# Performance work log

Hardware: AMD Instinct MI355X
Metric: run time of the kernel (lower is better)

The kernel has to match this reference:

```python
import jax, jax.numpy as jnp
import numpy as np


def _orthogonalize(Wfree):
    # Wfree: (S, C, C) free parameters -> batched QR with sign correction
    Q, R = jnp.linalg.qr(Wfree)
    s = jnp.sign(jnp.diagonal(R, axis1=-2, axis2=-1))  # (S, C)
    s = jnp.where(s == 0, jnp.ones_like(s), s)
    return Q * s[:, None, :]  # column-wise sign fix


def _channel_mix(x, Wfree):
    # x: (B, C, H, W); Wfree: (H*W, C, C)
    B, C, H, Wd = x.shape
    S = H * Wd
    Q = _orthogonalize(Wfree)                      # (S, C, C)
    xr = x.reshape(B, C, S).transpose(0, 2, 1)     # (B, S, C)
    # y[b,s,:] = x[b,s,:] @ Q[s].T  (matches torch matmul(x, Q.T))
    y = jnp.einsum('bsk,sck->bsc', xr, Q)
    return y.transpose(0, 2, 1).reshape(B, C, H, Wd)


def setup_inputs() -> dict:
    key = jax.random.key(0)
    k0, k1, k2, k3 = jax.random.split(key, 4)
    init_scale = 0.001
    x0 = jax.random.normal(k0, (32, 64, 28, 28), dtype=jnp.float32)
    x1 = jax.random.normal(k1, (32, 256, 14, 14), dtype=jnp.float32)
    W0 = jax.random.normal(k2, (28 * 28, 64, 64), dtype=jnp.float32) * init_scale
    W1 = jax.random.normal(k3, (14 * 14, 256, 256), dtype=jnp.float32) * init_scale
    return {"x0": x0, "x1": x1, "W0": W0, "W1": W1}


def reference(x0, x1, W0, W1):
    # C=64 and C=256 are perfect squares, so channel padding is a no-op.
    y0 = _channel_mix(x0, W0)
    y1 = _channel_mix(x1, W1)
    return (y0, y1)
```

## Files before the change

### kernel.cpp

```cpp
#include <hip/hip_runtime.h>


static constexpr int BB = 32;

#define SCHED_FENCE() __builtin_amdgcn_sched_barrier(0)

template<int CTRL>
__device__ __forceinline__ float dpp_add(float x) {
    int y = __builtin_amdgcn_update_dpp(0, __float_as_int(x), CTRL, 0xF, 0xF, false);
    return x + __int_as_float(y);
}
__device__ __forceinline__ float rowred16(float p) {
    p = dpp_add<0x128>(p);
    p = dpp_add<0x124>(p);
    p = dpp_add<0x122>(p);
    p = dpp_add<0x121>(p);
    return p;
}

__device__ __forceinline__ int qoff(int j, int g, int r16) {
    return j * 256 + g * 64 + ((r16 ^ (2 * g)) << 2);
}

__global__ __launch_bounds__(256) void tkern(const float* __restrict__ in,
                                             float* __restrict__ out,
                                             int R, int S) {
    __shared__ float tile[32][33];
    const int tx = threadIdx.x, ty = threadIdx.y;
    const int s0 = blockIdx.x * 32, r0 = blockIdx.y * 32;
    #pragma unroll
    for (int i = ty; i < 32; i += 8) {
        int r = r0 + i, s = s0 + tx;
        tile[i][tx] = (r < R && s < S) ? in[(size_t)r * S + s] : 0.f;
    }
    __syncthreads();
    #pragma unroll
    for (int i = ty; i < 32; i += 8) {
        int s = s0 + i, r = r0 + tx;
        if (s < S && r < R) out[(size_t)s * R + r] = tile[tx][i];
    }
}

template<int C, int CT, int KC>
__device__ __forceinline__ void qr_body(const float* __restrict__ W,
                                        float* __restrict__ XY,
                                        float* __restrict__ sm, int t) {
    constexpr int RT = 16;
    constexpr int TR = C / RT;
    constexpr int THREADS = RT * CT;
    constexpr int QSTR = TR + 4;
    constexpr int XSTR = C + 4;

    float* qs = sm;
    float* xs = sm + 2 * RT * QSTR;
    float* qc = xs + BB * XSTR;

    const int rb = t & 15;
    const int cb = t >> 4;

    float a[TR][4];
    {
        const float* Wp = W + (size_t)(rb * TR) * C + cb * 4;
        #pragma unroll
        for (int i = 0; i < TR; ++i) {
            float4 v = *reinterpret_cast<const float4*>(Wp + (size_t)i * C);
            a[i][0] = v.x; a[i][1] = v.y; a[i][2] = v.z; a[i][3] = v.w;
        }
    }
    {
        #pragma unroll
        for (int v = 0; v < (BB * C) / (4 * THREADS); ++v) {
            int idx = 4 * (t + v * THREADS);
            int b = idx / C, k = idx % C;
            float4 x4 = *reinterpret_cast<const float4*>(XY + idx);
            *reinterpret_cast<float4*>(&xs[b * XSTR + k]) = x4;
        }
    }

    int buf = 0;
    #pragma unroll 1
    for (int j = 0; j < C; ++j) {
        const int cbj = j >> 2, jj = j & 3;
        if (cb == cbj) {
            #pragma unroll
            for (int q = 0; q < 4; ++q) {
                if (q == jj) {
                    float p = 0.f;
                    #pragma unroll
                    for (int i = 0; i < TR; ++i) p += a[i][q] * a[i][q];
                    p = rowred16(p);
                    const float rn = 1.0f / sqrtf(p);
                    #pragma unroll
                    for (int i = 0; i < TR; ++i) a[i][q] *= rn;
                    #pragma unroll
                    for (int i = 0; i < TR; i += 4) {
                        *reinterpret_cast<float4*>(&qs[buf * RT * QSTR + rb * QSTR + i]) =
                            make_float4(a[i][q], a[i+1][q], a[i+2][q], a[i+3][q]);
                    }
                }
            }
        }
        __syncthreads();
        if (cb * 4 + 3 > j) {
            float qv[TR];
            #pragma unroll
            for (int i = 0; i < TR; i += 4) {
                float4 v = *reinterpret_cast<const float4*>(&qs[buf * RT * QSTR + rb * QSTR + i]);
                qv[i] = v.x; qv[i+1] = v.y; qv[i+2] = v.z; qv[i+3] = v.w;
            }
            #pragma unroll
            for (int q = 0; q < 4; ++q) {
                if (cb * 4 + q > j) {
                    float p = 0.f;
                    #pragma unroll
                    for (int i = 0; i < TR; ++i) p += a[i][q] * qv[i];
                    p = rowred16(p);
                    #pragma unroll
                    for (int i = 0; i < TR; ++i) a[i][q] -= p * qv[i];
                }
            }
        }
        buf ^= 1;
    }

    const int u  = t % (C / 4);
    const int bp = t / (C / 4);
    float acc[2][4] = {{0,0,0,0},{0,0,0,0}};

    #pragma unroll 1
    for (int ch = 0; ch < C / KC; ++ch) {
        __syncthreads();
        if (cb >= (ch * KC) / 4 && cb < ((ch + 1) * KC) / 4) {
            #pragma unroll
            for (int q = 0; q < 4; ++q) {
                const int kk = cb * 4 + q - ch * KC;
                const int swz = (kk & 7) << 2;
                #pragma unroll
                for (int i = 0; i < TR; i += 4) {
                    const int cout = rb * TR + i;
                    *reinterpret_cast<float4*>(&qc[kk * C + (cout ^ swz)]) =
                        make_float4(a[i][q], a[i+1][q], a[i+2][q], a[i+3][q]);
                }
            }
        }
        __syncthreads();
        #pragma unroll
        for (int kk = 0; kk < KC; kk += 4) {
            const int k = ch * KC + kk;
            float4 x0 = *reinterpret_cast<const float4*>(&xs[(2*bp    ) * XSTR + k]);
            float4 x1 = *reinterpret_cast<const float4*>(&xs[(2*bp + 1) * XSTR + k]);
            #pragma unroll
            for (int m = 0; m < 4; ++m) {
                const int swz = ((kk + m) & 7) << 2;
                float4 qv4 = *reinterpret_cast<const float4*>(&qc[(kk + m) * C + ((4 * u) ^ swz)]);
                const float xa = (&x0.x)[m], xb = (&x1.x)[m];
                acc[0][0] += xa * qv4.x; acc[0][1] += xa * qv4.y;
                acc[0][2] += xa * qv4.z; acc[0][3] += xa * qv4.w;
                acc[1][0] += xb * qv4.x; acc[1][1] += xb * qv4.y;
                acc[1][2] += xb * qv4.z; acc[1][3] += xb * qv4.w;
            }
        }
    }
    {
        *reinterpret_cast<float4*>(XY + (2*bp    ) * C + 4 * u) =
            make_float4(acc[0][0], acc[0][1], acc[0][2], acc[0][3]);
        *reinterpret_cast<float4*>(XY + (2*bp + 1) * C + 4 * u) =
            make_float4(acc[1][0], acc[1][1], acc[1][2], acc[1][3]);
    }
}

__device__ __forceinline__ void dot_upd(float (&a)[2][16], const float* qpan,
                                        int j, int rb) {
    const float4 q40 = *reinterpret_cast<const float4*>(&qpan[qoff(j, 0, rb)]);
    const float4 q41 = *reinterpret_cast<const float4*>(&qpan[qoff(j, 1, rb)]);
    const float4 q42 = *reinterpret_cast<const float4*>(&qpan[qoff(j, 2, rb)]);
    const float4 q43 = *reinterpret_cast<const float4*>(&qpan[qoff(j, 3, rb)]);
    float p0 = 0.f, p1 = 0.f;
    p0 += a[0][ 0]*q40.x; p1 += a[1][ 0]*q40.x;
    p0 += a[0][ 1]*q40.y; p1 += a[1][ 1]*q40.y;
    p0 += a[0][ 2]*q40.z; p1 += a[1][ 2]*q40.z;
    p0 += a[0][ 3]*q40.w; p1 += a[1][ 3]*q40.w;
    p0 += a[0][ 4]*q41.x; p1 += a[1][ 4]*q41.x;
    p0 += a[0][ 5]*q41.y; p1 += a[1][ 5]*q41.y;
    p0 += a[0][ 6]*q41.z; p1 += a[1][ 6]*q41.z;
    p0 += a[0][ 7]*q41.w; p1 += a[1][ 7]*q41.w;
    p0 += a[0][ 8]*q42.x; p1 += a[1][ 8]*q42.x;
    p0 += a[0][ 9]*q42.y; p1 += a[1][ 9]*q42.y;
    p0 += a[0][10]*q42.z; p1 += a[1][10]*q42.z;
    p0 += a[0][11]*q42.w; p1 += a[1][11]*q42.w;
    p0 += a[0][12]*q43.x; p1 += a[1][12]*q43.x;
    p0 += a[0][13]*q43.y; p1 += a[1][13]*q43.y;
    p0 += a[0][14]*q43.z; p1 += a[1][14]*q43.z;
    p0 += a[0][15]*q43.w; p1 += a[1][15]*q43.w;
    p0 = rowred16(p0); p1 = rowred16(p1);
    a[0][ 0] -= p0*q40.x; a[0][ 1] -= p0*q40.y;
    a[0][ 2] -= p0*q40.z; a[0][ 3] -= p0*q40.w;
    a[0][ 4] -= p0*q41.x; a[0][ 5] -= p0*q41.y;
    a[0][ 6] -= p0*q41.z; a[0][ 7] -= p0*q41.w;
    a[0][ 8] -= p0*q42.x; a[0][ 9] -= p0*q42.y;
    a[0][10] -= p0*q42.z; a[0][11] -= p0*q42.w;
    a[0][12] -= p0*q43.x; a[0][13] -= p0*q43.y;
    a[0][14] -= p0*q43.z; a[0][15] -= p0*q43.w;
    a[1][ 0] -= p1*q40.x; a[1][ 1] -= p1*q40.y;
    a[1][ 2] -= p1*q40.z; a[1][ 3] -= p1*q40.w;
    a[1][ 4] -= p1*q41.x; a[1][ 5] -= p1*q41.y;
    a[1][ 6] -= p1*q41.z; a[1][ 7] -= p1*q41.w;
    a[1][ 8] -= p1*q42.x; a[1][ 9] -= p1*q42.y;
    a[1][10] -= p1*q42.z; a[1][11] -= p1*q42.w;
    a[1][12] -= p1*q43.x; a[1][13] -= p1*q43.y;
    a[1][14] -= p1*q43.z; a[1][15] -= p1*q43.w;
}

__device__ __forceinline__ void mini_mgs2(float (&a)[2][16], float* qpan,
                                          int jx, int rb) {
    float p = 0.f;
    #pragma unroll
    for (int i = 0; i < 16; ++i) p += a[0][i] * a[0][i];
    p = rowred16(p);
    float rn = 1.0f / sqrtf(p);
    #pragma unroll
    for (int i = 0; i < 16; ++i) a[0][i] *= rn;
    #pragma unroll
    for (int g = 0; g < 4; ++g) {
        *reinterpret_cast<float4*>(&qpan[qoff(jx, g, rb)]) =
            make_float4(a[0][4*g], a[0][4*g+1], a[0][4*g+2], a[0][4*g+3]);
    }
    float q = 0.f;
    #pragma unroll
    for (int i = 0; i < 16; ++i) q += a[1][i] * a[0][i];
    q = rowred16(q);
    #pragma unroll
    for (int i = 0; i < 16; ++i) a[1][i] -= q * a[0][i];
    p = 0.f;
    #pragma unroll
    for (int i = 0; i < 16; ++i) p += a[1][i] * a[1][i];
    p = rowred16(p);
    rn = 1.0f / sqrtf(p);
    #pragma unroll
    for (int i = 0; i < 16; ++i) a[1][i] *= rn;
    #pragma unroll
    for (int g = 0; g < 4; ++g) {
        *reinterpret_cast<float4*>(&qpan[qoff(jx + 1, g, rb)]) =
            make_float4(a[1][4*g], a[1][4*g+1], a[1][4*g+2], a[1][4*g+3]);
    }
}

__device__ void panel_mgs(float (&a)[2][16], float* qpan, int rb, int cb) {
    if (cb == 0) mini_mgs2(a, qpan, 0, rb);
    __syncthreads();
    #pragma unroll 1
    for (int m = 0; m < 63; ++m) {
        if (cb > m) {
            dot_upd(a, qpan, 2*m,     rb);
            SCHED_FENCE();
            dot_upd(a, qpan, 2*m + 1, rb);
            SCHED_FENCE();
            if (cb == m + 1) mini_mgs2(a, qpan, 2*m + 2, rb);
        }
        __syncthreads();
    }
}

static constexpr int XST2 = 132;

__device__ __forceinline__ void apply_panel(float (&y0)[4], float (&y1)[4],
                                            const float* qpan, const float* xsb,
                                            int u, int v) {
    #pragma unroll 1
    for (int j4 = 0; j4 < 128; j4 += 4) {
        float4 xa4 = *reinterpret_cast<const float4*>(&xsb[(2*v    ) * XST2 + j4]);
        float4 xb4 = *reinterpret_cast<const float4*>(&xsb[(2*v + 1) * XST2 + j4]);
        #pragma unroll
        for (int m = 0; m < 4; ++m) {
            const int j = j4 + m;
            float4 q4 = *reinterpret_cast<const float4*>(&qpan[qoff(j, u & 3, u >> 2)]);
            const float xa = (&xa4.x)[m], xb = (&xb4.x)[m];
            y0[0] += xa*q4.x; y0[1] += xa*q4.y; y0[2] += xa*q4.z; y0[3] += xa*q4.w;
            y1[0] += xb*q4.x; y1[1] += xb*q4.y; y1[2] += xb*q4.z; y1[3] += xb*q4.w;
        }
    }
}

__device__ __forceinline__ void qr256_site(const float* __restrict__ Wp,
                                           float* __restrict__ Xp,
                                           float* __restrict__ sm, int t) {
    float* qpan = sm;
    float* xsb  = sm + 32768;

    const int rb = t & 15;
    const int cb = t >> 4;
    const int u  = t & 63;
    const int v  = t >> 6;

    float a[2][16];
    float y0[4] = {0,0,0,0};
    float y1[4] = {0,0,0,0};

    #pragma unroll
    for (int i = 0; i < 16; ++i) {
        float2 w2 = *reinterpret_cast<const float2*>(
            Wp + (size_t)(rb*16 + i) * 256 + 2*cb);
        a[0][i] = w2.x; a[1][i] = w2.y;
    }
    #pragma unroll
    for (int p = 0; p < 4; ++p) {
        const int idx = t + p * 1024;
        const int b = idx >> 7, jj = idx & 127;
        xsb[b * XST2 + jj] = Xp[b * 256 + jj];
    }
    panel_mgs(a, qpan, rb, cb);

    apply_panel(y0, y1, qpan, xsb, u, v);
    __syncthreads();

    #pragma unroll
    for (int i = 0; i < 16; ++i) {
        float2 w2 = *reinterpret_cast<const float2*>(
            Wp + (size_t)(rb*16 + i) * 256 + 128 + 2*cb);
        a[0][i] = w2.x; a[1][i] = w2.y;
    }
    #pragma unroll
    for (int p = 0; p < 4; ++p) {
        const int idx = t + p * 1024;
        const int b = idx >> 7, jj = idx & 127;
        xsb[b * XST2 + jj] = Xp[b * 256 + 128 + jj];
    }
    #pragma unroll 1
    for (int k = 0; k < 128; ++k) {
        dot_upd(a, qpan, k, rb);
        SCHED_FENCE();
    }
    __syncthreads();

    panel_mgs(a, qpan, rb, cb);
    apply_panel(y0, y1, qpan, xsb, u, v);

    *reinterpret_cast<float4*>(Xp + (size_t)(2*v    )*256 + 4*u) =
        make_float4(y0[0], y0[1], y0[2], y0[3]);
    *reinterpret_cast<float4*>(Xp + (size_t)(2*v + 1)*256 + 4*u) =
        make_float4(y1[0], y1[1], y1[2], y1[3]);
}

static constexpr int SM64 = 2*16*8 + 32*68 + 64*64;

__global__ __launch_bounds__(1024) void qr_all(const float* __restrict__ W0,
                                               const float* __restrict__ W1,
                                               float* __restrict__ XY0,
                                               float* __restrict__ XY1) {
    __shared__ float sm[32768 + 32 * XST2];
    const int bid = blockIdx.x;
    const int t   = threadIdx.x;
    if (bid < 196) {
        qr256_site(W1 + (size_t)bid * 65536, XY1 + (size_t)bid * 8192, sm, t);
    } else {
        const int sl = t >> 8;
        const int tt = t & 255;
        float* smL = sm + sl * SM64;
        #pragma unroll 1
        for (int uu = bid - 196; uu < 196; uu += 60) {
            const int site = 4 * uu + sl;
            qr_body<64, 16, 64>(W0 + (size_t)site * 4096,
                                XY0 + (size_t)site * 2048, smL, tt);
            __syncthreads();
        }
    }
}

extern "C" void kernel_launch(void* const* d_in, const int* in_sizes, int n_in,
                              void* d_out, int out_size, void* d_ws, size_t ws_size,
                              hipStream_t stream) {
    (void)in_sizes; (void)n_in; (void)out_size; (void)ws_size;
    const float* x0 = (const float*)d_in[0];
    const float* x1 = (const float*)d_in[1];
    const float* W0 = (const float*)d_in[2];
    const float* W1 = (const float*)d_in[3];
    float* y0  = (float*)d_out;
    float* y1  = y0 + 1605632;
    float* xt0 = (float*)d_ws;
    float* xt1 = xt0 + 1605632;

    dim3 tb(32, 8);
    tkern<<<dim3(25,  64), tb, 0, stream>>>(x0, xt0, 2048, 784);
    tkern<<<dim3(7,  256), tb, 0, stream>>>(x1, xt1, 8192, 196);
    qr_all<<<256, 1024, 0, stream>>>(W0, W1, xt0, xt1);
    tkern<<<dim3(64,  25), tb, 0, stream>>>(xt0, y0, 784, 2048);
    tkern<<<dim3(256,  7), tb, 0, stream>>>(xt1, y1, 196, 8192);
}
```

Measured before the change: 253.6 us.

## Block MGS panel by 8-column quads to cut barrier count

The panel Gram-Schmidt loop previously advanced two columns per step and issued a block-wide barrier after each of 63 steps. It now groups four 2-column slices into a wavefront-sized quad that is orthogonalized locally in sequence, then applies 8 projections per step, so only 15 barriers are needed. The intent is to reduce synchronization and serialization overhead in the QR. In exchange, more serial work runs inside one wave per step, and the three other waves of a quad wait on intra-quad dependencies without a barrier. That relies on the quad being a single wavefront.

Measured after the change: 290.3 us. 14.5% more time.

```diff
diff --git a/kernel.cpp b/kernel.cpp
--- a/kernel.cpp
+++ b/kernel.cpp
@@ -245,17 +245,45 @@
     }
 }
 
+__device__ __forceinline__ void retire_quad(float (&a)[2][16], float* qpan,
+                                            int base, int rb, int gi) {
+    if (gi == 0) mini_mgs2(a, qpan, base + 0, rb);
+    SCHED_FENCE();
+    if (gi >= 1) {
+        dot_upd(a, qpan, base + 0, rb); SCHED_FENCE();
+        dot_upd(a, qpan, base + 1, rb);
+    }
+    SCHED_FENCE();
+    if (gi == 1) mini_mgs2(a, qpan, base + 2, rb);
+    SCHED_FENCE();
+    if (gi >= 2) {
+        dot_upd(a, qpan, base + 2, rb); SCHED_FENCE();
+        dot_upd(a, qpan, base + 3, rb);
+    }
+    SCHED_FENCE();
+    if (gi == 2) mini_mgs2(a, qpan, base + 4, rb);
+    SCHED_FENCE();
+    if (gi == 3) {
+        dot_upd(a, qpan, base + 4, rb); SCHED_FENCE();
+        dot_upd(a, qpan, base + 5, rb); SCHED_FENCE();
+        mini_mgs2(a, qpan, base + 6, rb);
+    }
+}
+
 __device__ void panel_mgs(float (&a)[2][16], float* qpan, int rb, int cb) {
-    if (cb == 0) mini_mgs2(a, qpan, 0, rb);
+    const int wv = cb >> 2;
+    const int gi = cb & 3;
+    if (wv == 0) retire_quad(a, qpan, 0, rb, gi);
     __syncthreads();
     #pragma unroll 1
-    for (int m = 0; m < 63; ++m) {
-        if (cb > m) {
-            dot_upd(a, qpan, 2*m,     rb);
-            SCHED_FENCE();
-            dot_upd(a, qpan, 2*m + 1, rb);
-            SCHED_FENCE();
-            if (cb == m + 1) mini_mgs2(a, qpan, 2*m + 2, rb);
+    for (int m = 0; m < 15; ++m) {
+        if (wv > m) {
+            #pragma unroll 1
+            for (int jj = 0; jj < 8; ++jj) {
+                dot_upd(a, qpan, 8*m + jj, rb);
+                SCHED_FENCE();
+            }
+            if (wv == m + 1) retire_quad(a, qpan, 8*(m+1), rb, gi);
         }
         __syncthreads();
     }
```
